# Kernel tuning notes

Measured on AMD Instinct MI355X. Metric: run time of the kernel, lower is better.

Reference implementation:

```python
import jax, jax.numpy as jnp
import numpy as np
import math

# B queries, N complex ambient dim, M codebook entries, S payload dim, K quad nodes
B, N, M, S, K = 1024, 128, 8192, 256, 8
EPS_TOTAL = 1e-3
OVERLAP, ANISO = 0.25, 0.75
_t, _w = np.polynomial.hermite.hermgauss(K)
GH_T = jnp.asarray(_t, jnp.float32)
GH_W = jnp.asarray(_w, jnp.float32)


def _init_sigmas():
    # mirrors CPSFFusedCodebook._init_sigmas (log-space for numerical safety at N=128)
    rho = 1.0 + ANISO
    logV = (N / 2.0) * math.log(math.pi) - math.lgamma(N / 2.0 + 1.0)
    log_r = (math.log(OVERLAP) - math.log(M) - logV - math.log(rho)) / N
    r_perp = math.exp(log_r)
    s_perp = 2.0 * math.pi * r_perp ** 2
    return rho * rho * s_perp, s_perp


def setup_inputs() -> dict:
    key = jax.random.key(0)
    ks = jax.random.split(key, 12)
    u = lambda k, sh: jax.random.uniform(k, sh, jnp.float32, -1.0, 1.0)
    s_par, s_perp = _init_sigmas()
    return {
        "z_re": u(ks[0], (B, N)), "z_im": u(ks[1], (B, N)),
        "d_re": u(ks[2], (B, N)), "d_im": u(ks[3], (B, N)),
        "zj_re": 0.5 * u(ks[4], (M, N)), "zj_im": 0.5 * u(ks[5], (M, N)),
        "dj_re": 0.5 * u(ks[6], (M, N)), "dj_im": 0.5 * u(ks[7], (M, N)),
        "T_re": u(ks[8], (M, S)), "T_im": u(ks[9], (M, S)),
        "alpha": jax.random.uniform(ks[10], (M,), jnp.float32, 0.5, 1.5),
        "sigma_par": jnp.full((M,), s_par, jnp.float32),
        "sigma_perp": jnp.full((M,), s_perp, jnp.float32),
    }


def _unit(xr, xi):
    n = jnp.sqrt(jnp.sum(xr * xr + xi * xi, -1, keepdims=True))
    n = jnp.where(n == 0, jnp.ones_like(n), n)
    return xr / n, xi / n


def _forward(z_re, z_im, d_re, d_im, zj_re, zj_im, dj_re, dj_im,
             T_re, T_im, alpha, sigma_par, sigma_perp):
    tiny = jnp.float32(np.finfo(np.float32).tiny)
    dur, dui = _unit(d_re, d_im)          # autonorm_vec_d
    djr, dji = _unit(dj_re, dj_im)        # autonorm_vec_d_j
    a = jnp.maximum(alpha, tiny)
    sp = jnp.maximum(sigma_par, tiny)
    sq = jnp.maximum(sigma_perp, tiny)

    # proj[b,m] = <d_j, z - z_j> (conj-linear in d_j); all via GEMMs, no [B,M,N] tensor
    pr = z_re @ djr.T + z_im @ dji.T - jnp.sum(djr * zj_re + dji * zj_im, -1)[None, :]
    pi = z_im @ djr.T - z_re @ dji.T - jnp.sum(djr * zj_im - dji * zj_re, -1)[None, :]

    # |z - z_j|^2 via GEMM expansion
    dz2 = (jnp.sum(z_re * z_re + z_im * z_im, -1)[:, None]
           + jnp.sum(zj_re * zj_re + zj_im * zj_im, -1)[None, :]
           - 2.0 * (z_re @ zj_re.T + z_im @ zj_im.T))
    perp2 = jnp.maximum(dz2 - (pr * pr + pi * pi), 0.0)  # component orthogonal to d_j

    # Gauss-Hermite quadrature along the codebook direction, scaled per-code
    scale = jnp.sqrt(sp / jnp.pi)                     # [M]
    t = GH_T[None, :] * scale[:, None]                # [M,K] quad offsets
    par2 = (pr[:, :, None] - t[None]) ** 2 + (pi * pi)[:, :, None]   # [B,M,K]
    env = jnp.exp(-jnp.pi * (par2 / sp[None, :, None]
                             + (perp2 / sq[None, :])[:, :, None]))
    rho = jnp.einsum('bmk,k->bm', env, GH_W) * (scale / jnp.sqrt(jnp.pi))[None, :]

    # angular alignment |<d_j, d>|^2
    ar = dur @ djr.T + dui @ dji.T
    ai = dui @ djr.T - dur @ dji.T
    align = ar * ar + ai * ai

    w = a[None, :] * align * rho                      # [B,M] real mixture weights
    den = jnp.sum(w, -1) + EPS_TOTAL                  # [B]
    out_re = (w @ T_re) / den[:, None]                # [B,S]
    out_im = (w @ T_im) / den[:, None]
    return jnp.stack([out_re, out_im], -1)            # [B,S,2] == complex [B,S]


def reference(z_re, z_im, d_re, d_im, zj_re, zj_im, dj_re, dj_im,
              T_re, T_im, alpha, sigma_par, sigma_perp):
    return _forward(z_re, z_im, d_re, d_im, zj_re, zj_im, dj_re, dj_im,
                    T_re, T_im, alpha, sigma_par, sigma_perp)
```

## Files before the change

### kernel.cpp

```cpp
#include <hip/hip_runtime.h>
#include <math.h>

#define Bq 1024
#define Nn 128
#define Mm 8192
#define Ss 256

typedef _Float16 f16;
typedef _Float16 f16x8 __attribute__((ext_vector_type(8)));
typedef _Float16 f16x4 __attribute__((ext_vector_type(4)));
typedef float f32x4 __attribute__((ext_vector_type(4)));

#define PI_F 3.14159265358979323846f
#define INV_SQRT_PI 0.5641895835477563f
#define TINY_F 1.17549435e-38f
#define EPS_TOTAL 1e-3f
#define WSC 1024.0f

#define GLOAD16(g, l) \
    __builtin_amdgcn_global_load_lds((const __attribute__((address_space(1))) void*)(g), \
                                     (__attribute__((address_space(3))) void*)(l), 16, 0, 0)

__global__ void cpsf_prep_all(const float* __restrict__ z_re, const float* __restrict__ z_im,
                              const float* __restrict__ d_re, const float* __restrict__ d_im,
                              const float* __restrict__ zj_re, const float* __restrict__ zj_im,
                              const float* __restrict__ dj_re, const float* __restrict__ dj_im,
                              const float* __restrict__ alpha, const float* __restrict__ sp_,
                              const float* __restrict__ sq_, float* __restrict__ z2,
                              float* __restrict__ cm, f16* __restrict__ Az)
{
    const int wid = threadIdx.x >> 6;
    const int l = threadIdx.x & 63;
    if (blockIdx.x < 256) {
        const int b = blockIdx.x * 4 + wid;
        const int o = b * Nn;
        float dr0 = d_re[o + l], dr1 = d_re[o + l + 64];
        float di0 = d_im[o + l], di1 = d_im[o + l + 64];
        float zr0 = z_re[o + l], zr1 = z_re[o + l + 64];
        float zi0 = z_im[o + l], zi1 = z_im[o + l + 64];
        float sd = dr0*dr0 + di0*di0 + dr1*dr1 + di1*di1;
        float sz = zr0*zr0 + zi0*zi0 + zr1*zr1 + zi1*zi1;
#pragma unroll
        for (int off = 1; off < 64; off <<= 1) {
            sd += __shfl_xor(sd, off);
            sz += __shfl_xor(sz, off);
        }
        float nd = sqrtf(sd);
        nd = (nd == 0.0f) ? 1.0f : nd;
        float inv = 1.0f / nd;
        if (l == 0) z2[b] = sz;
        int map = l >> 5, c = l & 31;
        int k8 = (c & 15) * 8;
        const float* src = (map == 0) ? ((c < 16) ? z_re : z_im)
                                      : ((c < 16) ? d_re : d_im);
        float s = (map == 0) ? 1.0f : inv;
        float4 v0 = *(const float4*)(src + (size_t)b * Nn + k8);
        float4 v1 = *(const float4*)(src + (size_t)b * Nn + k8 + 4);
        f16x8 ov = {(f16)(v0.x*s), (f16)(v0.y*s), (f16)(v0.z*s), (f16)(v0.w*s),
                    (f16)(v1.x*s), (f16)(v1.y*s), (f16)(v1.z*s), (f16)(v1.w*s)};
        *(f16x8*)(Az + ((size_t)l * 1024 + b) * 8) = ov;
    } else {
        const int m = (blockIdx.x - 256) * 4 + wid;
        const int o = m * Nn;
        float dr0 = dj_re[o + l], dr1 = dj_re[o + l + 64];
        float di0 = dj_im[o + l], di1 = dj_im[o + l + 64];
        float zr0 = zj_re[o + l], zr1 = zj_re[o + l + 64];
        float zi0 = zj_im[o + l], zi1 = zj_im[o + l + 64];
        float snd = dr0*dr0 + di0*di0 + dr1*dr1 + di1*di1;
        float sc1 = dr0*zr0 + di0*zi0 + dr1*zr1 + di1*zi1;
        float sc2 = dr0*zi0 - di0*zr0 + dr1*zi1 - di1*zr1;
        float sz2 = zr0*zr0 + zi0*zi0 + zr1*zr1 + zi1*zi1;
#pragma unroll
        for (int off = 1; off < 64; off <<= 1) {
            snd += __shfl_xor(snd, off);
            sc1 += __shfl_xor(sc1, off);
            sc2 += __shfl_xor(sc2, off);
            sz2 += __shfl_xor(sz2, off);
        }
        if (l == 0) {
            float nd = sqrtf(snd);
            nd = (nd == 0.0f) ? 1.0f : nd;
            float inv = 1.0f / nd;
            cm[0*Mm + m] = inv;
            cm[1*Mm + m] = sc1 * inv;
            cm[2*Mm + m] = sc2 * inv;
            cm[3*Mm + m] = sz2;
            float sp = fmaxf(sp_[m], TINY_F);
            float sq = fmaxf(sq_[m], TINY_F);
            float sc = sqrtf(sp / PI_F);
            cm[4*Mm + m] = PI_F / sp;
            cm[5*Mm + m] = PI_F / sq;
            cm[6*Mm + m] = fmaxf(alpha[m], TINY_F) * sc * INV_SQRT_PI;
            cm[7*Mm + m] = sc;
        }
    }
}

__global__ void cpsf_pack_b1(const float* __restrict__ zj_re, const float* __restrict__ zj_im,
                             const float* __restrict__ dj_re, const float* __restrict__ dj_im,
                             f16* __restrict__ Bp, int Mc, int m0g, int mshift)
{
    int idx = blockIdx.x * 256 + threadIdx.x;
    int m = idx & (Mc - 1);
    int pc = idx >> mshift;
    int p = pc >> 5, c = pc & 31;
    int mg = m0g + m;
    int hi = (c >= 16);
    int k8 = (c & 15) * 8;
    const float* src;
    float sgn = 1.0f;
    if (p == 0)      src = hi ? dj_im : dj_re;
    else if (p == 1) { src = hi ? dj_re : dj_im; sgn = hi ? 1.0f : -1.0f; }
    else             src = hi ? zj_im : zj_re;
    float4 v0 = *(const float4*)(src + (size_t)mg * Nn + k8);
    float4 v1 = *(const float4*)(src + (size_t)mg * Nn + k8 + 4);
    f16x8 o = {(f16)(v0.x*sgn), (f16)(v0.y*sgn), (f16)(v0.z*sgn), (f16)(v0.w*sgn),
               (f16)(v1.x*sgn), (f16)(v1.y*sgn), (f16)(v1.z*sgn), (f16)(v1.w*sgn)};
    *(f16x8*)(Bp + (size_t)idx * 8) = o;
}

__global__ void cpsf_pack_tt(const float* __restrict__ T_re, const float* __restrict__ T_im,
                             f16* __restrict__ Tt, int Mc, int m0g)
{
    __shared__ float tr[64][65], ti[64][65];
    const int mb = blockIdx.x * 64, sb = blockIdx.y * 64;
    const int tid = threadIdx.x;
    const int i0 = tid >> 6, j = tid & 63;
#pragma unroll
    for (int it = 0; it < 16; ++it) {
        int i = it * 4 + i0;
        tr[i][j] = T_re[(size_t)(m0g + mb + i) * Ss + sb + j];
        ti[i][j] = T_im[(size_t)(m0g + mb + i) * Ss + sb + j];
    }
    __syncthreads();
#pragma unroll
    for (int it = 0; it < 16; ++it) {
        int jj = it * 4 + i0;
        int sp = (sb + jj) * 2;
        Tt[(size_t)sp * Mc + mb + j]       = (f16)tr[j][jj];
        Tt[(size_t)(sp + 1) * Mc + mb + j] = (f16)ti[j][jj];
    }
}

__global__ __launch_bounds__(256, 2) void cpsf_gemm_w(
    const f16* __restrict__ Az, const f16* __restrict__ Bp,
    const float* __restrict__ cm, const float* __restrict__ z2v,
    f16* __restrict__ wbuf, float* __restrict__ den, int Mc, int m0g)
{
    const int tid = threadIdx.x;
    const int wid = tid >> 6;
    const int lane = tid & 63;
    const int q = lane >> 4;
    const int li = lane & 15;

    const int nmt = gridDim.x;
    const int sbid = blockIdx.x + nmt * blockIdx.y;
    const int xcd = sbid & 7;
    const int j = sbid >> 3;
    const int mpg = nmt >> 3;
    const int mtile = xcd * mpg + (j & (mpg - 1));
    const int btile = j / mpg;
    const int mb0 = mtile * 64;
    const int bb0 = btile * 128;
    const int wb0 = (wid >> 1) * 64;
    const int wm0 = (wid & 1) * 32;

    const f16* pAz = Az + ((size_t)(q) * 1024 + bb0 + wb0 + li) * 8;
    const f16* pAu = pAz + (size_t)32 * 1024 * 8;
    const f16* pB0 = Bp + ((size_t)(0 * 32 + q) * Mc + mb0 + wm0 + li) * 8;
    const f16* pB1 = Bp + ((size_t)(1 * 32 + q) * Mc + mb0 + wm0 + li) * 8;
    const f16* pB2 = Bp + ((size_t)(2 * 32 + q) * Mc + mb0 + wm0 + li) * 8;
    const size_t KSA = (size_t)4 * 1024 * 8;
    const size_t KSB = (size_t)4 * Mc * 8;

    f32x4 accP[4][2][3];
    f32x4 accQ[4][2][2];
#pragma unroll
    for (int t = 0; t < 4; ++t)
#pragma unroll
        for (int u = 0; u < 2; ++u) {
#pragma unroll
            for (int p = 0; p < 3; ++p) accP[t][u][p] = (f32x4){0.f,0.f,0.f,0.f};
#pragma unroll
            for (int p = 0; p < 2; ++p) accQ[t][u][p] = (f32x4){0.f,0.f,0.f,0.f};
        }

    f16x8 azA[4], auA[4], bfA[6], azB[4], auB[4], bfB[6];

#define LOADSET(AZ, AU, BF, KS) do {                                              \
    const size_t oA = (size_t)(KS) * KSA;                                         \
    const size_t oB = (size_t)(KS) * KSB;                                         \
    AZ[0] = *(const f16x8*)(pAz + oA);        AZ[1] = *(const f16x8*)(pAz + oA + 128); \
    AZ[2] = *(const f16x8*)(pAz + oA + 256);  AZ[3] = *(const f16x8*)(pAz + oA + 384); \
    AU[0] = *(const f16x8*)(pAu + oA);        AU[1] = *(const f16x8*)(pAu + oA + 128); \
    AU[2] = *(const f16x8*)(pAu + oA + 256);  AU[3] = *(const f16x8*)(pAu + oA + 384); \
    BF[0] = *(const f16x8*)(pB0 + oB);        BF[1] = *(const f16x8*)(pB0 + oB + 128); \
    BF[2] = *(const f16x8*)(pB1 + oB);        BF[3] = *(const f16x8*)(pB1 + oB + 128); \
    BF[4] = *(const f16x8*)(pB2 + oB);        BF[5] = *(const f16x8*)(pB2 + oB + 128); \
} while (0)

#define MFMASET(AZ, AU, BF) do {                                                  \
    _Pragma("unroll")                                                             \
    for (int t = 0; t < 4; ++t)                                                   \
        _Pragma("unroll")                                                         \
        for (int u = 0; u < 2; ++u) {                                             \
            accP[t][u][0] = __builtin_amdgcn_mfma_f32_16x16x32_f16(AZ[t], BF[0*2+u], accP[t][u][0], 0, 0, 0); \
            accP[t][u][1] = __builtin_amdgcn_mfma_f32_16x16x32_f16(AZ[t], BF[1*2+u], accP[t][u][1], 0, 0, 0); \
            accP[t][u][2] = __builtin_amdgcn_mfma_f32_16x16x32_f16(AZ[t], BF[2*2+u], accP[t][u][2], 0, 0, 0); \
            accQ[t][u][0] = __builtin_amdgcn_mfma_f32_16x16x32_f16(AU[t], BF[0*2+u], accQ[t][u][0], 0, 0, 0); \
            accQ[t][u][1] = __builtin_amdgcn_mfma_f32_16x16x32_f16(AU[t], BF[1*2+u], accQ[t][u][1], 0, 0, 0); \
        }                                                                         \
} while (0)

    LOADSET(azA, auA, bfA, 0);
#pragma unroll
    for (int kk = 0; kk < 4; ++kk) {
        LOADSET(azB, auB, bfB, kk * 2 + 1);
        MFMASET(azA, auA, bfA);
        if (kk < 3) LOADSET(azA, auA, bfA, kk * 2 + 2);
        MFMASET(azB, auB, bfB);
    }
#undef LOADSET
#undef MFMASET

    const float GT[8] = {-2.9306374202572440f, -1.9816567566958429f,
                         -1.1571937124467802f, -0.3811869902073221f,
                          0.3811869902073221f,  1.1571937124467802f,
                          1.9816567566958429f,  2.9306374202572440f};
    const float GW[8] = {1.9960407221136762e-04f, 1.7077983007413475e-02f,
                         2.0780232581489188e-01f, 6.6114701255824129e-01f,
                         6.6114701255824129e-01f, 2.0780232581489188e-01f,
                         1.7077983007413475e-02f, 1.9960407221136762e-04f};

    float iv[2], c1[2], c2[2], zj2[2], isp[2], isq[2], cf[2], scl[2];
#pragma unroll
    for (int u = 0; u < 2; ++u) {
        int mg = m0g + mb0 + wm0 + u * 16 + li;
        iv[u]  = cm[0*Mm + mg];
        c1[u]  = cm[1*Mm + mg];  c2[u]  = cm[2*Mm + mg];
        zj2[u] = cm[3*Mm + mg];  isp[u] = cm[4*Mm + mg];
        isq[u] = cm[5*Mm + mg];  cf[u]  = cm[6*Mm + mg];
        scl[u] = cm[7*Mm + mg];
    }

    float dsum[4][4];
#pragma unroll
    for (int t = 0; t < 4; ++t)
#pragma unroll
        for (int r = 0; r < 4; ++r) dsum[t][r] = 0.f;

#pragma unroll
    for (int t = 0; t < 4; ++t) {
#pragma unroll
        for (int r = 0; r < 4; ++r) {
            const int b = bb0 + wb0 + t * 16 + q * 4 + r;
            const float z2b = z2v[b];
#pragma unroll
            for (int u = 0; u < 2; ++u) {
                float pr = accP[t][u][0][r] * iv[u] - c1[u];
                float pi = accP[t][u][1][r] * iv[u] - c2[u];
                float dz2 = z2b + zj2[u] - 2.0f * accP[t][u][2][r];
                float perp2 = fmaxf(dz2 - pr * pr - pi * pi, 0.0f);
                float base = -(isq[u] * perp2 + isp[u] * pi * pi);
                float rho = 0.0f;
#pragma unroll
                for (int k = 0; k < 8; ++k) {
                    float dd = pr - scl[u] * GT[k];
                    rho = fmaf(GW[k], __expf(base - isp[u] * dd * dd), rho);
                }
                float ar = accQ[t][u][0][r] * iv[u], ai = accQ[t][u][1][r] * iv[u];
                float wv = cf[u] * (ar * ar + ai * ai) * rho;
                dsum[t][r] += wv;
                wbuf[(size_t)b * Mc + mb0 + wm0 + u * 16 + li] = (f16)(wv * WSC);
            }
        }
    }
#pragma unroll
    for (int t = 0; t < 4; ++t)
#pragma unroll
        for (int r = 0; r < 4; ++r) {
            float v = dsum[t][r];
            v += __shfl_xor(v, 1);
            v += __shfl_xor(v, 2);
            v += __shfl_xor(v, 4);
            v += __shfl_xor(v, 8);
            if (li == 0) atomicAdd(den + bb0 + wb0 + t * 16 + q * 4 + r, v);
        }
}

__global__ __launch_bounds__(256, 3) void cpsf_gemm_out(
    const f16* __restrict__ wbuf, const f16* __restrict__ Tt,
    float* __restrict__ oacc, int Mc, int Kw)
{
    __shared__ __align__(16) f16 sm[2 * 1024 * 8];
    const int tid = threadIdx.x;
    const int wid = tid >> 6;
    const int lane = tid & 63;
    const int q = lane >> 4;
    const int li = lane & 15;
    const int sb0 = blockIdx.x * 128;
    const int bb0 = blockIdx.y * 128;
    const int kz0 = blockIdx.z * Kw;
    const int wb0 = (wid >> 1) * 64;
    const int ws0 = (wid & 1) * 64;
    const int BUFO = 1024 * 8;

    const f16* gp[4];
    f16* lb[4];
#pragma unroll
    for (int i = 0; i < 4; ++i) {
        int c = i * 4 + wid;
        const f16* src;
        if (c < 8) {
            int g = c >> 1, row = (c & 1) * 64 + lane;
            src = wbuf + (size_t)(bb0 + row) * Mc + kz0 + g * 8;
        } else {
            int c2 = c - 8;
            int g = c2 >> 1, row = (c2 & 1) * 64 + lane;
            src = Tt + (size_t)(sb0 + row) * Mc + kz0 + g * 8;
        }
        gp[i] = src;
        lb[i] = sm + (size_t)(i * 256 + wid * 64) * 8;
    }

    f32x4 acc[4][4];
#pragma unroll
    for (int t = 0; t < 4; ++t)
#pragma unroll
        for (int u = 0; u < 4; ++u) acc[t][u] = (f32x4){0.f,0.f,0.f,0.f};

#pragma unroll
    for (int i = 0; i < 4; ++i) {
        GLOAD16(gp[i], lb[i]);
        gp[i] += 32;
    }
    __syncthreads();

    const int nk = Kw >> 5;
    for (int kc = 0; kc < nk; ++kc) {
        const int buf = kc & 1;
        if (kc + 1 < nk) {
#pragma unroll
            for (int i = 0; i < 4; ++i) {
                GLOAD16(gp[i], lb[i] + (buf ^ 1) * BUFO);
                gp[i] += 32;
            }
        }
        const f16* bs = sm + buf * BUFO;
        f16x8 af[4], bf[4];
#pragma unroll
        for (int t = 0; t < 4; ++t)
            af[t] = *(const f16x8*)(bs + (size_t)(q * 128 + wb0 + t * 16 + li) * 8);
#pragma unroll
        for (int u = 0; u < 4; ++u)
            bf[u] = *(const f16x8*)(bs + (size_t)(512 + q * 128 + ws0 + u * 16 + li) * 8);
#pragma unroll
        for (int t = 0; t < 4; ++t)
#pragma unroll
            for (int u = 0; u < 4; ++u)
                acc[t][u] = __builtin_amdgcn_mfma_f32_16x16x32_f16(af[t], bf[u], acc[t][u], 0, 0, 0);
        __syncthreads();
    }
#pragma unroll
    for (int t = 0; t < 4; ++t)
#pragma unroll
        for (int u = 0; u < 4; ++u)
#pragma unroll
            for (int r = 0; r < 4; ++r)
                atomicAdd(oacc + (size_t)(bb0 + wb0 + t * 16 + q * 4 + r) * 512 + sb0 + ws0 + u * 16 + li,
                          acc[t][u][r]);
}

__global__ void cpsf_fin(const float* __restrict__ oacc, const float* __restrict__ den,
                         float* __restrict__ out)
{
    int i = blockIdx.x * 256 + threadIdx.x;
    float d = (den[i >> 9] + EPS_TOTAL) * WSC;
    out[i] = oacc[i] / d;
}

extern "C" void kernel_launch(void* const* d_in, const int* in_sizes, int n_in,
                              void* d_out, int out_size, void* d_ws, size_t ws_size,
                              hipStream_t stream)
{
    (void)in_sizes; (void)n_in; (void)out_size;
    const float* z_re  = (const float*)d_in[0];
    const float* z_im  = (const float*)d_in[1];
    const float* d_re  = (const float*)d_in[2];
    const float* d_im  = (const float*)d_in[3];
    const float* zj_re = (const float*)d_in[4];
    const float* zj_im = (const float*)d_in[5];
    const float* dj_re = (const float*)d_in[6];
    const float* dj_im = (const float*)d_in[7];
    const float* T_re  = (const float*)d_in[8];
    const float* T_im  = (const float*)d_in[9];
    const float* alpha = (const float*)d_in[10];
    const float* s_par = (const float*)d_in[11];
    const float* s_perp= (const float*)d_in[12];

    char* w8 = (char*)d_ws;
    const size_t o_out  = 0;
    const size_t o_den  = o_out + (size_t)Bq * 512 * 4;
    const size_t o_z2   = o_den + 4096;
    const size_t o_cm   = o_z2 + 4096;
    const size_t o_az   = o_cm + (size_t)8 * Mm * 4;
    const size_t o_ch   = o_az + (size_t)Bq * 512 * 2;
    int Mc = 512;
    if      (o_ch + (size_t)4608 * 8192 <= ws_size) Mc = 8192;
    else if (o_ch + (size_t)4608 * 4096 <= ws_size) Mc = 4096;
    else if (o_ch + (size_t)4608 * 2048 <= ws_size) Mc = 2048;
    else if (o_ch + (size_t)4608 * 1024 <= ws_size) Mc = 1024;
    int mshift = 31 - __builtin_clz((unsigned)Mc);
    int zs = Mc / 512; if (zs < 1) zs = 1;
    int Kw = Mc / zs;

    float* oacc = (float*)(w8 + o_out);
    float* den  = (float*)(w8 + o_den);
    float* z2   = (float*)(w8 + o_z2);
    float* cm   = (float*)(w8 + o_cm);
    f16*   Az   = (f16*)(w8 + o_az);
    f16*   Bp   = (f16*)(w8 + o_ch);
    f16*   Tt   = (f16*)(w8 + o_ch + (size_t)1536 * Mc);
    f16*   wb   = (f16*)(w8 + o_ch + (size_t)2560 * Mc);

    hipMemsetAsync(d_ws, 0, o_z2, stream);

    cpsf_prep_all<<<256 + Mm / 4, 256, 0, stream>>>(z_re, z_im, d_re, d_im,
                                                    zj_re, zj_im, dj_re, dj_im,
                                                    alpha, s_par, s_perp, z2, cm, Az);

    for (int m0 = 0; m0 < Mm; m0 += Mc) {
        cpsf_pack_b1<<<(96 * Mc) / 256, 256, 0, stream>>>(zj_re, zj_im, dj_re, dj_im,
                                                          Bp, Mc, m0, mshift);
        cpsf_pack_tt<<<dim3(Mc / 64, Ss / 64), 256, 0, stream>>>(T_re, T_im, Tt, Mc, m0);
        cpsf_gemm_w<<<dim3(Mc / 64, Bq / 128), 256, 0, stream>>>(Az, Bp, cm, z2, wb, den, Mc, m0);
        cpsf_gemm_out<<<dim3(4, Bq / 128, zs), 256, 0, stream>>>(wb, Tt, oacc, Mc, Kw);
    }
    cpsf_fin<<<(Bq * 512) / 256, 256, 0, stream>>>(oacc, den, (float*)d_out);
}
```

Measured before the change: 260.6 us.

## Fuse prep/pack kernels, LDS-pipeline gemm_w, replace atomics with split-K slices

Merges the prep, B-pack and T-transpose kernels into one launch per chunk to cut launch overhead. The first GEMM now stages operands through double-buffered LDS using global_load_lds, with explicit waitcnt, barriers and setprio, in place of direct register loads. The output GEMM writes per-split-K slices instead of atomicAdd, and the final kernel sums those slices, which drops the large memset. This trades more workspace and extra reduction reads for avoiding atomic contention.

```diff
diff --git a/kernel.cpp b/kernel.cpp
--- a/kernel.cpp
+++ b/kernel.cpp
@@ -21,18 +21,25 @@
     __builtin_amdgcn_global_load_lds((const __attribute__((address_space(1))) void*)(g), \
                                      (__attribute__((address_space(3))) void*)(l), 16, 0, 0)
 
-__global__ void cpsf_prep_all(const float* __restrict__ z_re, const float* __restrict__ z_im,
-                              const float* __restrict__ d_re, const float* __restrict__ d_im,
-                              const float* __restrict__ zj_re, const float* __restrict__ zj_im,
-                              const float* __restrict__ dj_re, const float* __restrict__ dj_im,
-                              const float* __restrict__ alpha, const float* __restrict__ sp_,
-                              const float* __restrict__ sq_, float* __restrict__ z2,
-                              float* __restrict__ cm, f16* __restrict__ Az)
+__global__ void cpsf_prep_pack(
+    const float* __restrict__ z_re, const float* __restrict__ z_im,
+    const float* __restrict__ d_re, const float* __restrict__ d_im,
+    const float* __restrict__ zj_re, const float* __restrict__ zj_im,
+    const float* __restrict__ dj_re, const float* __restrict__ dj_im,
+    const float* __restrict__ T_re, const float* __restrict__ T_im,
+    const float* __restrict__ alpha, const float* __restrict__ sp_,
+    const float* __restrict__ sq_, float* __restrict__ z2,
+    float* __restrict__ cm, f16* __restrict__ Az, f16* __restrict__ Bp,
+    f16* __restrict__ Tt, int Mc, int m0g, int n0, int n1, int n2, int mshift)
 {
-    const int wid = threadIdx.x >> 6;
-    const int l = threadIdx.x & 63;
-    if (blockIdx.x < 256) {
-        const int b = blockIdx.x * 4 + wid;
+    __shared__ float tsm[2 * 64 * 65];
+    const int bx = blockIdx.x;
+    const int tid = threadIdx.x;
+    const int wid = tid >> 6;
+    const int l = tid & 63;
+
+    if (bx < n0) {
+        const int b = bx * 4 + wid;
         const int o = b * Nn;
         float dr0 = d_re[o + l], dr1 = d_re[o + l + 64];
         float di0 = d_im[o + l], di1 = d_im[o + l + 64];
@@ -59,8 +66,8 @@
         f16x8 ov = {(f16)(v0.x*s), (f16)(v0.y*s), (f16)(v0.z*s), (f16)(v0.w*s),
                     (f16)(v1.x*s), (f16)(v1.y*s), (f16)(v1.z*s), (f16)(v1.w*s)};
         *(f16x8*)(Az + ((size_t)l * 1024 + b) * 8) = ov;
-    } else {
-        const int m = (blockIdx.x - 256) * 4 + wid;
+    } else if (bx < n0 + n1) {
+        const int m = (bx - n0) * 4 + wid;
         const int o = m * Nn;
         float dr0 = dj_re[o + l], dr1 = dj_re[o + l + 64];
         float di0 = dj_im[o + l], di1 = dj_im[o + l + 64];
@@ -93,52 +100,45 @@
             cm[6*Mm + m] = fmaxf(alpha[m], TINY_F) * sc * INV_SQRT_PI;
             cm[7*Mm + m] = sc;
         }
-    }
-}
-
-__global__ void cpsf_pack_b1(const float* __restrict__ zj_re, const float* __restrict__ zj_im,
-                             const float* __restrict__ dj_re, const float* __restrict__ dj_im,
-                             f16* __restrict__ Bp, int Mc, int m0g, int mshift)
-{
-    int idx = blockIdx.x * 256 + threadIdx.x;
-    int m = idx & (Mc - 1);
-    int pc = idx >> mshift;
-    int p = pc >> 5, c = pc & 31;
-    int mg = m0g + m;
-    int hi = (c >= 16);
-    int k8 = (c & 15) * 8;
-    const float* src;
-    float sgn = 1.0f;
-    if (p == 0)      src = hi ? dj_im : dj_re;
-    else if (p == 1) { src = hi ? dj_re : dj_im; sgn = hi ? 1.0f : -1.0f; }
-    else             src = hi ? zj_im : zj_re;
-    float4 v0 = *(const float4*)(src + (size_t)mg * Nn + k8);
-    float4 v1 = *(const float4*)(src + (size_t)mg * Nn + k8 + 4);
-    f16x8 o = {(f16)(v0.x*sgn), (f16)(v0.y*sgn), (f16)(v0.z*sgn), (f16)(v0.w*sgn),
-               (f16)(v1.x*sgn), (f16)(v1.y*sgn), (f16)(v1.z*sgn), (f16)(v1.w*sgn)};
-    *(f16x8*)(Bp + (size_t)idx * 8) = o;
-}
-
-__global__ void cpsf_pack_tt(const float* __restrict__ T_re, const float* __restrict__ T_im,
-                             f16* __restrict__ Tt, int Mc, int m0g)
-{
-    __shared__ float tr[64][65], ti[64][65];
-    const int mb = blockIdx.x * 64, sb = blockIdx.y * 64;
-    const int tid = threadIdx.x;
-    const int i0 = tid >> 6, j = tid & 63;
-#pragma unroll
-    for (int it = 0; it < 16; ++it) {
-        int i = it * 4 + i0;
-        tr[i][j] = T_re[(size_t)(m0g + mb + i) * Ss + sb + j];
-        ti[i][j] = T_im[(size_t)(m0g + mb + i) * Ss + sb + j];
-    }
-    __syncthreads();
-#pragma unroll
-    for (int it = 0; it < 16; ++it) {
-        int jj = it * 4 + i0;
-        int sp = (sb + jj) * 2;
-        Tt[(size_t)sp * Mc + mb + j]       = (f16)tr[j][jj];
-        Tt[(size_t)(sp + 1) * Mc + mb + j] = (f16)ti[j][jj];
+    } else if (bx < n0 + n1 + n2) {
+        int idx = (bx - n0 - n1) * 256 + tid;
+        int m = idx & (Mc - 1);
+        int pc = idx >> mshift;
+        int p = pc >> 5, c = pc & 31;
+        int mg = m0g + m;
+        int hi = (c >= 16);
+        int k8 = (c & 15) * 8;
+        const float* src;
+        float sgn = 1.0f;
+        if (p == 0)      src = hi ? dj_im : dj_re;
+        else if (p == 1) { src = hi ? dj_re : dj_im; sgn = hi ? 1.0f : -1.0f; }
+        else             src = hi ? zj_im : zj_re;
+        float4 v0 = *(const float4*)(src + (size_t)mg * Nn + k8);
+        float4 v1 = *(const float4*)(src + (size_t)mg * Nn + k8 + 4);
+        f16x8 o = {(f16)(v0.x*sgn), (f16)(v0.y*sgn), (f16)(v0.z*sgn), (f16)(v0.w*sgn),
+                   (f16)(v1.x*sgn), (f16)(v1.y*sgn), (f16)(v1.z*sgn), (f16)(v1.w*sgn)};
+        *(f16x8*)(Bp + (size_t)idx * 8) = o;
+    } else {
+        const int bt = bx - n0 - n1 - n2;
+        const int nmb = Mc >> 6;
+        const int mb = (bt & (nmb - 1)) * 64, sb = (bt / nmb) * 64;
+        float* tr = tsm;
+        float* ti = tsm + 64 * 65;
+        const int i0 = tid >> 6, jj0 = tid & 63;
+#pragma unroll
+        for (int it = 0; it < 16; ++it) {
+            int i = it * 4 + i0;
+            tr[i * 65 + jj0] = T_re[(size_t)(m0g + mb + i) * Ss + sb + jj0];
+            ti[i * 65 + jj0] = T_im[(size_t)(m0g + mb + i) * Ss + sb + jj0];
+        }
+        __syncthreads();
+#pragma unroll
+        for (int it = 0; it < 16; ++it) {
+            int jj = it * 4 + i0;
+            int sp = (sb + jj) * 2;
+            Tt[(size_t)sp * Mc + mb + jj0]       = (f16)tr[jj0 * 65 + jj];
+            Tt[(size_t)(sp + 1) * Mc + mb + jj0] = (f16)ti[jj0 * 65 + jj];
+        }
     }
 }
 
@@ -147,6 +147,7 @@
     const float* __restrict__ cm, const float* __restrict__ z2v,
     f16* __restrict__ wbuf, float* __restrict__ den, int Mc, int m0g)
 {
+    __shared__ __align__(16) f16 sm[2 * 1792 * 8];
     const int tid = threadIdx.x;
     const int wid = tid >> 6;
     const int lane = tid & 63;
@@ -156,22 +157,42 @@
     const int nmt = gridDim.x;
     const int sbid = blockIdx.x + nmt * blockIdx.y;
     const int xcd = sbid & 7;
-    const int j = sbid >> 3;
+    const int jb = sbid >> 3;
     const int mpg = nmt >> 3;
-    const int mtile = xcd * mpg + (j & (mpg - 1));
-    const int btile = j / mpg;
+    const int mtile = xcd * mpg + (jb & (mpg - 1));
+    const int btile = jb / mpg;
     const int mb0 = mtile * 64;
     const int bb0 = btile * 128;
     const int wb0 = (wid >> 1) * 64;
     const int wm0 = (wid & 1) * 32;
-
-    const f16* pAz = Az + ((size_t)(q) * 1024 + bb0 + wb0 + li) * 8;
-    const f16* pAu = pAz + (size_t)32 * 1024 * 8;
-    const f16* pB0 = Bp + ((size_t)(0 * 32 + q) * Mc + mb0 + wm0 + li) * 8;
-    const f16* pB1 = Bp + ((size_t)(1 * 32 + q) * Mc + mb0 + wm0 + li) * 8;
-    const f16* pB2 = Bp + ((size_t)(2 * 32 + q) * Mc + mb0 + wm0 + li) * 8;
-    const size_t KSA = (size_t)4 * 1024 * 8;
-    const size_t KSB = (size_t)4 * Mc * 8;
+    const int BUFO = 1792 * 8;
+
+    const f16* gp[7];
+    size_t gstep[7];
+    f16* lb[7];
+#pragma unroll
+    for (int i = 0; i < 7; ++i) {
+        int c = i * 4 + wid;
+        const f16* src;
+        size_t st;
+        if (c < 8) {
+            int g = c >> 1, row = (c & 1) * 64 + lane;
+            src = Az + ((size_t)g * 1024 + bb0 + row) * 8;
+            st = (size_t)4 * 1024 * 8;
+        } else if (c < 16) {
+            int c2 = c - 8;
+            int g = c2 >> 1, row = (c2 & 1) * 64 + lane;
+            src = Az + ((size_t)(32 + g) * 1024 + bb0 + row) * 8;
+            st = (size_t)4 * 1024 * 8;
+        } else {
+            int c2 = c - 16;
+            int g = c2 / 3, p = c2 % 3;
+            src = Bp + ((size_t)(p * 32 + g) * Mc + mb0 + lane) * 8;
+            st = (size_t)4 * Mc * 8;
+        }
+        gp[i] = src; gstep[i] = st;
+        lb[i] = sm + (size_t)(i * 256 + wid * 64) * 8;
+    }
 
     f32x4 accP[4][2][3];
     f32x4 accQ[4][2][2];
@@ -185,43 +206,53 @@
             for (int p = 0; p < 2; ++p) accQ[t][u][p] = (f32x4){0.f,0.f,0.f,0.f};
         }
 
-    f16x8 azA[4], auA[4], bfA[6], azB[4], auB[4], bfB[6];
-
-#define LOADSET(AZ, AU, BF, KS) do {                                              \
-    const size_t oA = (size_t)(KS) * KSA;                                         \
-    const size_t oB = (size_t)(KS) * KSB;                                         \
-    AZ[0] = *(const f16x8*)(pAz + oA);        AZ[1] = *(const f16x8*)(pAz + oA + 128); \
-    AZ[2] = *(const f16x8*)(pAz + oA + 256);  AZ[3] = *(const f16x8*)(pAz + oA + 384); \
-    AU[0] = *(const f16x8*)(pAu + oA);        AU[1] = *(const f16x8*)(pAu + oA + 128); \
-    AU[2] = *(const f16x8*)(pAu + oA + 256);  AU[3] = *(const f16x8*)(pAu + oA + 384); \
-    BF[0] = *(const f16x8*)(pB0 + oB);        BF[1] = *(const f16x8*)(pB0 + oB + 128); \
-    BF[2] = *(const f16x8*)(pB1 + oB);        BF[3] = *(const f16x8*)(pB1 + oB + 128); \
-    BF[4] = *(const f16x8*)(pB2 + oB);        BF[5] = *(const f16x8*)(pB2 + oB + 128); \
-} while (0)
-
-#define MFMASET(AZ, AU, BF) do {                                                  \
-    _Pragma("unroll")                                                             \
-    for (int t = 0; t < 4; ++t)                                                   \
-        _Pragma("unroll")                                                         \
-        for (int u = 0; u < 2; ++u) {                                             \
-            accP[t][u][0] = __builtin_amdgcn_mfma_f32_16x16x32_f16(AZ[t], BF[0*2+u], accP[t][u][0], 0, 0, 0); \
-            accP[t][u][1] = __builtin_amdgcn_mfma_f32_16x16x32_f16(AZ[t], BF[1*2+u], accP[t][u][1], 0, 0, 0); \
-            accP[t][u][2] = __builtin_amdgcn_mfma_f32_16x16x32_f16(AZ[t], BF[2*2+u], accP[t][u][2], 0, 0, 0); \
-            accQ[t][u][0] = __builtin_amdgcn_mfma_f32_16x16x32_f16(AU[t], BF[0*2+u], accQ[t][u][0], 0, 0, 0); \
-            accQ[t][u][1] = __builtin_amdgcn_mfma_f32_16x16x32_f16(AU[t], BF[1*2+u], accQ[t][u][1], 0, 0, 0); \
-        }                                                                         \
-} while (0)
-
-    LOADSET(azA, auA, bfA, 0);
-#pragma unroll
-    for (int kk = 0; kk < 4; ++kk) {
-        LOADSET(azB, auB, bfB, kk * 2 + 1);
-        MFMASET(azA, auA, bfA);
-        if (kk < 3) LOADSET(azA, auA, bfA, kk * 2 + 2);
-        MFMASET(azB, auB, bfB);
-    }
-#undef LOADSET
-#undef MFMASET
+#pragma unroll
+    for (int i = 0; i < 7; ++i) { GLOAD16(gp[i], lb[i]); gp[i] += gstep[i]; }
+
+#pragma unroll
+    for (int ks = 0; ks < 8; ++ks) {
+        const int p = ks & 1;
+        if (ks > 0) {
+            __builtin_amdgcn_sched_barrier(0);
+            __builtin_amdgcn_s_barrier();
+        }
+        if (ks < 7) {
+#pragma unroll
+            for (int i = 0; i < 7; ++i) { GLOAD16(gp[i], lb[i] + (p ^ 1) * BUFO); gp[i] += gstep[i]; }
+            asm volatile("s_waitcnt vmcnt(7)" ::: "memory");
+        } else {
+            asm volatile("s_waitcnt vmcnt(0)" ::: "memory");
+        }
+        __builtin_amdgcn_sched_barrier(0);
+        __builtin_amdgcn_s_barrier();
+
+        const f16* bs = sm + p * BUFO;
+        f16x8 az[4], au[4], bf[3][2];
+#pragma unroll
+        for (int t = 0; t < 4; ++t) {
+            az[t] = *(const f16x8*)(bs + (size_t)(q * 128 + wb0 + t * 16 + li) * 8);
+            au[t] = *(const f16x8*)(bs + (size_t)(512 + q * 128 + wb0 + t * 16 + li) * 8);
+        }
+#pragma unroll
+        for (int pp = 0; pp < 3; ++pp)
+#pragma unroll
+            for (int u = 0; u < 2; ++u)
+                bf[pp][u] = *(const f16x8*)(bs + (size_t)(1024 + q * 192 + pp * 64 + wm0 + u * 16 + li) * 8);
+
+        __builtin_amdgcn_s_setprio(1);
+#pragma unroll
+        for (int t = 0; t < 4; ++t)
+#pragma unroll
+            for (int u = 0; u < 2; ++u) {
+#pragma unroll
+                for (int pp = 0; pp < 3; ++pp)
+                    accP[t][u][pp] = __builtin_amdgcn_mfma_f32_16x16x32_f16(az[t], bf[pp][u], accP[t][u][pp], 0, 0, 0);
+#pragma unroll
+                for (int pp = 0; pp < 2; ++pp)
+                    accQ[t][u][pp] = __builtin_amdgcn_mfma_f32_16x16x32_f16(au[t], bf[pp][u], accQ[t][u][pp], 0, 0, 0);
+            }
+        __builtin_amdgcn_s_setprio(0);
+    }
 
     const float GT[8] = {-2.9306374202572440f, -1.9816567566958429f,
                          -1.1571937124467802f, -0.3811869902073221f,
@@ -290,7 +321,7 @@
 
 __global__ __launch_bounds__(256, 3) void cpsf_gemm_out(
     const f16* __restrict__ wbuf, const f16* __restrict__ Tt,
-    float* __restrict__ oacc, int Mc, int Kw)
+    float* __restrict__ osl, int Mc, int Kw)
 {
     __shared__ __align__(16) f16 sm[2 * 1024 * 8];
     const int tid = threadIdx.x;
@@ -301,6 +332,7 @@
     const int sb0 = blockIdx.x * 128;
     const int bb0 = blockIdx.y * 128;
     const int kz0 = blockIdx.z * Kw;
+    float* oz = osl + (size_t)blockIdx.z * ((size_t)Bq * 512);
     const int wb0 = (wid >> 1) * 64;
     const int ws0 = (wid & 1) * 64;
     const int BUFO = 1024 * 8;
@@ -330,23 +362,26 @@
         for (int u = 0; u < 4; ++u) acc[t][u] = (f32x4){0.f,0.f,0.f,0.f};
 
 #pragma unroll
-    for (int i = 0; i < 4; ++i) {
-        GLOAD16(gp[i], lb[i]);
-        gp[i] += 32;
-    }
-    __syncthreads();
+    for (int i = 0; i < 4; ++i) { GLOAD16(gp[i], lb[i]); gp[i] += 32; }
 
     const int nk = Kw >> 5;
     for (int kc = 0; kc < nk; ++kc) {
-        const int buf = kc & 1;
+        const int p = kc & 1;
+        if (kc > 0) {
+            __builtin_amdgcn_sched_barrier(0);
+            __builtin_amdgcn_s_barrier();
+        }
         if (kc + 1 < nk) {
 #pragma unroll
-            for (int i = 0; i < 4; ++i) {
-                GLOAD16(gp[i], lb[i] + (buf ^ 1) * BUFO);
-                gp[i] += 32;
-            }
-        }
-        const f16* bs = sm + buf * BUFO;
+            for (int i = 0; i < 4; ++i) { GLOAD16(gp[i], lb[i] + (p ^ 1) * BUFO); gp[i] += 32; }
+            asm volatile("s_waitcnt vmcnt(4)" ::: "memory");
+        } else {
+            asm volatile("s_waitcnt vmcnt(0)" ::: "memory");
+        }
+        __builtin_amdgcn_sched_barrier(0);
+        __builtin_amdgcn_s_barrier();
+
+        const f16* bs = sm + p * BUFO;
         f16x8 af[4], bf[4];
 #pragma unroll
         for (int t = 0; t < 4; ++t)
@@ -354,12 +389,13 @@
 #pragma unroll
         for (int u = 0; u < 4; ++u)
             bf[u] = *(const f16x8*)(bs + (size_t)(512 + q * 128 + ws0 + u * 16 + li) * 8);
+        __builtin_amdgcn_s_setprio(1);
 #pragma unroll
         for (int t = 0; t < 4; ++t)
 #pragma unroll
             for (int u = 0; u < 4; ++u)
                 acc[t][u] = __builtin_amdgcn_mfma_f32_16x16x32_f16(af[t], bf[u], acc[t][u], 0, 0, 0);
-        __syncthreads();
+        __builtin_amdgcn_s_setprio(0);
     }
 #pragma unroll
     for (int t = 0; t < 4; ++t)
@@ -367,16 +403,17 @@
         for (int u = 0; u < 4; ++u)
 #pragma unroll
             for (int r = 0; r < 4; ++r)
-                atomicAdd(oacc + (size_t)(bb0 + wb0 + t * 16 + q * 4 + r) * 512 + sb0 + ws0 + u * 16 + li,
-                          acc[t][u][r]);
+                oz[(size_t)(bb0 + wb0 + t * 16 + q * 4 + r) * 512 + sb0 + ws0 + u * 16 + li] =
+                    acc[t][u][r];
 }
 
-__global__ void cpsf_fin(const float* __restrict__ oacc, const float* __restrict__ den,
-                         float* __restrict__ out)
+__global__ void cpsf_fin(const float* __restrict__ osl, const float* __restrict__ den,
+                         float* __restrict__ out, int Z)
 {
     int i = blockIdx.x * 256 + threadIdx.x;
-    float d = (den[i >> 9] + EPS_TOTAL) * WSC;
-    out[i] = oacc[i] / d;
+    float s = 0.f;
+    for (int z = 0; z < Z; ++z) s += osl[(size_t)z * ((size_t)Bq * 512) + i];
+    out[i] = s / ((den[i >> 9] + EPS_TOTAL) * WSC);
 }
 
 extern "C" void kernel_launch(void* const* d_in, const int* in_sizes, int n_in,
@@ -398,43 +435,58 @@
     const float* s_par = (const float*)d_in[11];
     const float* s_perp= (const float*)d_in[12];
 
+    const size_t SL = (size_t)Bq * 512 * 4;
+    const size_t fixedA = 4096 + 4096 + (size_t)8 * Mm * 4 + (size_t)Bq * 512 * 2;
+
+    int Mc = 0, Z = 0;
+    const int Zopt[3] = {16, 8, 4};
+    const int Mopt[4] = {8192, 4096, 2048, 1024};
+    for (int zi = 0; zi < 3 && !Mc; ++zi)
+        for (int mi = 0; mi < 4; ++mi) {
+            int Zc = Zopt[zi], Mcc = Mopt[mi];
+            int nch = Mm / Mcc;
+            if (Zc % nch) continue;
+            size_t need = (size_t)Zc * SL + fixedA + (size_t)4608 * Mcc;
+            if (need <= ws_size) { Mc = Mcc; Z = Zc; break; }
+        }
+    if (!Mc) { Mc = 1024; Z = 8; }
+    const int nch = Mm / Mc;
+    const int zs = Z / nch;
+    const int Kw = Mc / zs;
+    const int mshift = 31 - __builtin_clz((unsigned)Mc);
+
     char* w8 = (char*)d_ws;
-    const size_t o_out  = 0;
-    const size_t o_den  = o_out + (size_t)Bq * 512 * 4;
-    const size_t o_z2   = o_den + 4096;
-    const size_t o_cm   = o_z2 + 4096;
-    const size_t o_az   = o_cm + (size_t)8 * Mm * 4;
-    const size_t o_ch   = o_az + (size_t)Bq * 512 * 2;
-    int Mc = 512;
-    if      (o_ch + (size_t)4608 * 8192 <= ws_size) Mc = 8192;
-    else if (o_ch + (size_t)4608 * 4096 <= ws_size) Mc = 4096;
-    else if (o_ch + (size_t)4608 * 2048 <= ws_size) Mc = 2048;
-    else if (o_ch + (size_t)4608 * 1024 <= ws_size) Mc = 1024;
-    int mshift = 31 - __builtin_clz((unsigned)Mc);
-    int zs = Mc / 512; if (zs < 1) zs = 1;
-    int Kw = Mc / zs;
-
-    float* oacc = (float*)(w8 + o_out);
-    float* den  = (float*)(w8 + o_den);
-    float* z2   = (float*)(w8 + o_z2);
-    float* cm   = (float*)(w8 + o_cm);
-    f16*   Az   = (f16*)(w8 + o_az);
-    f16*   Bp   = (f16*)(w8 + o_ch);
-    f16*   Tt   = (f16*)(w8 + o_ch + (size_t)1536 * Mc);
-    f16*   wb   = (f16*)(w8 + o_ch + (size_t)2560 * Mc);
-
-    hipMemsetAsync(d_ws, 0, o_z2, stream);
-
-    cpsf_prep_all<<<256 + Mm / 4, 256, 0, stream>>>(z_re, z_im, d_re, d_im,
-                                                    zj_re, zj_im, dj_re, dj_im,
-                                                    alpha, s_par, s_perp, z2, cm, Az);
-
-    for (int m0 = 0; m0 < Mm; m0 += Mc) {
-        cpsf_pack_b1<<<(96 * Mc) / 256, 256, 0, stream>>>(zj_re, zj_im, dj_re, dj_im,
-                                                          Bp, Mc, m0, mshift);
-        cpsf_pack_tt<<<dim3(Mc / 64, Ss / 64), 256, 0, stream>>>(T_re, T_im, Tt, Mc, m0);
-        cpsf_gemm_w<<<dim3(Mc / 64, Bq / 128), 256, 0, stream>>>(Az, Bp, cm, z2, wb, den, Mc, m0);
-        cpsf_gemm_out<<<dim3(4, Bq / 128, zs), 256, 0, stream>>>(wb, Tt, oacc, Mc, Kw);
-    }
-    cpsf_fin<<<(Bq * 512) / 256, 256, 0, stream>>>(oacc, den, (float*)d_out);
+    const size_t o_sl  = 0;
+    const size_t o_den = o_sl + (size_t)Z * SL;
+    const size_t o_z2  = o_den + 4096;
+    const size_t o_cm  = o_z2 + 4096;
+    const size_t o_az  = o_cm + (size_t)8 * Mm * 4;
+    const size_t o_ch  = o_az + (size_t)Bq * 512 * 2;
+
+    float* osl = (float*)(w8 + o_sl);
+    float* den = (float*)(w8 + o_den);
+    float* z2  = (float*)(w8 + o_z2);
+    float* cm  = (float*)(w8 + o_cm);
+    f16*   Az  = (f16*)(w8 + o_az);
+    f16*   Bp  = (f16*)(w8 + o_ch);
+    f16*   Tt  = (f16*)(w8 + o_ch + (size_t)1536 * Mc);
+    f16*   wb  = (f16*)(w8 + o_ch + (size_t)2560 * Mc);
+
+    hipMemsetAsync(w8 + o_den, 0, 4096, stream);
+
+    for (int ci = 0; ci < nch; ++ci) {
+        const int m0 = ci * Mc;
+        const int n0 = (ci == 0) ? 256 : 0;
+        const int n1 = (ci == 0) ? Mm / 4 : 0;
+        const int n2 = (96 * Mc) / 256;
+        const int n3 = (Mc / 64) * (Ss / 64);
+        cpsf_prep_pack<<<n0 + n1 + n2 + n3, 256, 0, stream>>>(
+            z_re, z_im, d_re, d_im, zj_re, zj_im, dj_re, dj_im, T_re, T_im,
+            alpha, s_par, s_perp, z2, cm, Az, Bp, Tt, Mc, m0, n0, n1, n2, mshift);
+        cpsf_gemm_w<<<dim3(Mc / 64, Bq / 128), 256, 0, stream>>>(
+            Az, Bp, cm, z2, wb, den, Mc, m0);
+        cpsf_gemm_out<<<dim3(4, Bq / 128, zs), 256, 0, stream>>>(
+            wb, Tt, osl + (size_t)ci * zs * ((size_t)Bq * 512), Mc, Kw);
+    }
+    cpsf_fin<<<(Bq * 512) / 256, 256, 0, stream>>>(osl, den, (float*)d_out, Z);
 }
```

Result: faster. 219.8 us (-15.7%).
